# Kernel tuning notes

Hardware: AMD Instinct MI355X
Metric: run time of the kernel (lower is better)

## Reference

```python
import jax, jax.numpy as jnp
import numpy as np

N = 131072   # total inner-graph nodes (G * n)
G = 2048     # number of inner graphs = nodes of outer graph fg
n = 64       # nodes per inner graph (contiguous blocks)
E = 1048576  # inner edges
EF = 32768   # outer (fg) edges
D = 128      # emb_dim == hidden_dim
K = 8        # SortPooling k
VOCAB = 150


def setup_inputs() -> dict:
    key = jax.random.key(0)
    ks = jax.random.split(key, 32)
    p = lambda k, shape: (jax.random.normal(k, shape, jnp.float32) * 0.1)
    inp = {
        'h': jax.random.randint(ks[0], (N,), 0, VOCAB),
        'g_src': jax.random.randint(ks[1], (E,), 0, N),
        'g_dst': jax.random.randint(ks[2], (E,), 0, N),
        'fg_src': jax.random.randint(ks[3], (EF,), 0, G),
        'fg_dst': jax.random.randint(ks[4], (EF,), 0, G),
        'token_emb': p(ks[5], (VOCAB, D)),
        # GATConv 1 (D -> D, 1 head): fc weight (in,out), attn vectors, output bias
        'W1': p(ks[6], (D, D)), 'al1': p(ks[7], (D,)), 'ar1': p(ks[8], (D,)), 'b1': p(ks[9], (D,)),
        # GATConv 2
        'W2': p(ks[10], (D, D)), 'al2': p(ks[11], (D,)), 'ar2': p(ks[12], (D,)), 'b2': p(ks[13], (D,)),
        # GATConv 3 (K*D -> D) over fg
        'W3': p(ks[14], (K * D, D)), 'al3': p(ks[15], (D,)), 'ar3': p(ks[16], (D,)), 'b3': p(ks[17], (D,)),
        # linear_forward
        'Wf': p(ks[18], (D, D)), 'bf': p(ks[19], (D,)),
        # linear
        'Wl': p(ks[20], (D, D)), 'bl': p(ks[21], (D,)),
        # linear1
        'Wl1': p(ks[22], (D, D)), 'bl1': p(ks[23], (D,)),
        # clasifier
        'Wc': p(ks[24], (D, 2)), 'bc': p(ks[25], (2,)),
    }
    return inp


def gat_conv(src, dst, num_nodes, x, W, al, ar, b):
    """DGL GATConv, num_heads=1, allow_zero_in_degree=True, no activation."""
    f = x @ W                                   # [N, D] projected features
    el = f @ al                                 # [N] left attention logits
    er = f @ ar                                 # [N] right attention logits
    e = jax.nn.leaky_relu(el[src] + er[dst], 0.2)   # [E] per-edge score
    m = jax.ops.segment_max(e, dst, num_segments=num_nodes)
    a = jnp.exp(e - m[dst])
    s = jax.ops.segment_sum(a, dst, num_segments=num_nodes)
    alpha = a / s[dst]                          # edge softmax over incoming edges
    out = jax.ops.segment_sum(alpha[:, None] * f[src], dst, num_segments=num_nodes)
    return out + b                              # zero-in-degree nodes -> bias only


def sort_pooling(x, num_graphs, nodes_per_graph, k):
    """DGL SortPooling: sort each node's feature ascending, rank nodes by last
    channel descending, take top-k, concat -> [G, k*D]."""
    d = x.shape[-1]
    x = jnp.sort(x.reshape(num_graphs, nodes_per_graph, d), axis=-1)
    idx = jnp.argsort(-x[:, :, -1], axis=1)[:, :k]          # [G, k]
    topk = jnp.take_along_axis(x, idx[:, :, None], axis=1)  # [G, k, D]
    return topk.reshape(num_graphs, k * d)


def reference(h, g_src, g_dst, fg_src, fg_dst, token_emb,
              W1, al1, ar1, b1, W2, al2, ar2, b2, W3, al3, ar3, b3,
              Wf, bf, Wl, bl, Wl1, bl1, Wc, bc):
    x = jax.nn.relu(token_emb[h])                                   # [N, D]
    x = jax.nn.relu(gat_conv(g_src, g_dst, N, x, W1, al1, ar1, b1))
    x = jax.nn.relu(gat_conv(g_src, g_dst, N, x, W2, al2, ar2, b2))
    x = jax.nn.relu(x @ Wf + bf)                                    # linear_forward
    x = sort_pooling(x, G, n, K)                                    # [G, K*D]
    x = jax.nn.relu(gat_conv(fg_src, fg_dst, G, x, W3, al3, ar3, b3))
    x = jax.nn.relu(x @ Wl + bl)                                    # dropout = eval identity
    x = jax.nn.relu(x @ Wl1 + bl1)
    x = x @ Wc + bc
    return x.reshape(-1, 2)
```

## Files before the change

### kernel.cpp

```cpp
#include <hip/hip_runtime.h>
#include <math.h>

#define NN   131072
#define GG   2048
#define NPG  64
#define EE   1048576
#define EFN  32768
#define DD   128
#define KK   8

typedef unsigned short bfu;
typedef short bf16x8 __attribute__((ext_vector_type(8)));
typedef float f32x4 __attribute__((ext_vector_type(4)));

static __device__ __forceinline__ bfu f2b(float f) {
  unsigned u = __float_as_uint(f);
  u += 0x7FFFu + ((u >> 16) & 1u);
  return (bfu)(u >> 16);
}
static __device__ __forceinline__ float b2f(bfu b) {
  return __uint_as_float(((unsigned)b) << 16);
}

__global__ void fill_f32_kernel(float* __restrict__ p, float v, int nElems) {
  int i = blockIdx.x * 256 + threadIdx.x;
  if (i < nElems) p[i] = v;
}

__global__ void zero_int_kernel(int* __restrict__ p, int nElems) {
  int i = blockIdx.x * 256 + threadIdx.x;
  if (i < nElems) p[i] = 0;
}

__global__ void init_softmax_kernel(float* __restrict__ mx, float* __restrict__ sm, int nElems) {
  int i = blockIdx.x * 256 + threadIdx.x;
  if (i < nElems) { mx[i] = -INFINITY; sm[i] = 0.f; }
}

__global__ void embed_relu_kernel(const float* __restrict__ temb,
                                  const int* __restrict__ h,
                                  float* __restrict__ x, int total) {
  int i = blockIdx.x * 256 + threadIdx.x;
  if (i >= total) return;
  int node = i >> 7, d = i & 127;
  x[i] = fmaxf(temb[h[node] * DD + d], 0.f);
}

template <int KD, int ROWS>
__global__ __launch_bounds__(128) void gemm_kernel(
    const float* __restrict__ A, const float* __restrict__ W,
    const float* __restrict__ bias, float* __restrict__ out,
    int relu_flag) {
  __shared__ float As[ROWS * KD];
  const int row0 = blockIdx.x * ROWS;
  const int tid = threadIdx.x;
  for (int i = tid; i < ROWS * KD; i += 128) As[i] = A[(size_t)row0 * KD + i];
  __syncthreads();
  float acc[ROWS];
#pragma unroll
  for (int r = 0; r < ROWS; r++) acc[r] = 0.f;
  for (int k = 0; k < KD; k++) {
    float w = W[k * 128 + tid];
#pragma unroll
    for (int r = 0; r < ROWS; r++) acc[r] += As[r * KD + k] * w;
  }
  float b = bias ? bias[tid] : 0.f;
#pragma unroll
  for (int r = 0; r < ROWS; r++) {
    float v = acc[r] + b;
    if (relu_flag) v = fmaxf(v, 0.f);
    out[(size_t)(row0 + r) * 128 + tid] = v;
  }
}

__global__ __launch_bounds__(256) void gemm1024_kernel(
    const float* __restrict__ A, const float* __restrict__ W,
    float* __restrict__ out) {
  __shared__ float As[8 * 1024];
  __shared__ float red[8][256];
  const int t = threadIdx.x;
  const int row0 = blockIdx.x * 8;
  for (int idx = t; idx < 8 * 256; idx += 256) {
    int r = idx >> 8, c4 = (idx & 255) << 2;
    *(float4*)&As[r * 1024 + c4] = *(const float4*)(A + (size_t)(row0 + r) * 1024 + c4);
  }
  __syncthreads();
  const int col = t & 127, kh = t >> 7;
  const int k0 = kh * 512;
  float acc[8];
#pragma unroll
  for (int r = 0; r < 8; r++) acc[r] = 0.f;
  for (int k = k0; k < k0 + 512; k += 4) {
    float w0 = W[(size_t)(k + 0) * 128 + col];
    float w1 = W[(size_t)(k + 1) * 128 + col];
    float w2 = W[(size_t)(k + 2) * 128 + col];
    float w3 = W[(size_t)(k + 3) * 128 + col];
#pragma unroll
    for (int r = 0; r < 8; r++) {
      float4 a = *(const float4*)&As[r * 1024 + k];
      acc[r] += a.x * w0 + a.y * w1 + a.z * w2 + a.w * w3;
    }
  }
#pragma unroll
  for (int r = 0; r < 8; r++) red[r][t] = acc[r];
  __syncthreads();
  for (int idx = t; idx < 1024; idx += 256) {
    int r = idx >> 7, c = idx & 127;
    out[(size_t)(row0 + r) * 128 + c] = red[r][c] + red[r][128 + c];
  }
}

__global__ void pack_w_kernel(const float* __restrict__ W,
                              bfu* __restrict__ hi, bfu* __restrict__ lo) {
  int i = blockIdx.x * 256 + threadIdx.x;
  if (i >= 16384) return;
  int k = i >> 7, n = i & 127;
  float w = W[i];
  bfu h = f2b(w);
  bfu l = f2b(w - b2f(h));
  int kk = k >> 5, k5 = k & 31, quad = k5 >> 3, j = k5 & 7;
  int tt = n >> 4, m16 = n & 15;
  int pos = ((((kk * 8 + tt) * 4 + quad) * 16) + m16) * 8 + j;
  hi[pos] = h;
  lo[pos] = l;
}

template <int SRC_MODE, int EPI>
__global__ __launch_bounds__(256) void mfma_gemm(
    const float* A, const float* __restrict__ temb,
    const int* __restrict__ hidx,
    const bfu* __restrict__ WfHi, const bfu* __restrict__ WfLo,
    const float* __restrict__ bias, void* out,
    const float* __restrict__ al, const float* __restrict__ ar,
    float* __restrict__ el, float* __restrict__ er,
    float* __restrict__ keyb) {
  const int t = threadIdx.x;
  const int lane = t & 63, wv_ = t >> 6;
  const int m16 = lane & 15, quad = lane >> 4;
  const int rowbase = blockIdx.x * 64 + wv_ * 16;
  const int grow = rowbase + m16;
  const float* arow = (SRC_MODE == 1) ? (temb + (size_t)hidx[grow] * 128)
                                      : (A + (size_t)grow * 128);
  f32x4 acc[8];
#pragma unroll
  for (int i = 0; i < 8; i++) acc[i] = (f32x4){0.f, 0.f, 0.f, 0.f};
#pragma unroll
  for (int kk = 0; kk < 4; kk++) {
    int k0 = kk * 32 + quad * 8;
    float av[8];
    *(float4*)&av[0] = *(const float4*)(arow + k0);
    *(float4*)&av[4] = *(const float4*)(arow + k0 + 4);
    if (SRC_MODE == 1) {
#pragma unroll
      for (int i = 0; i < 8; i++) av[i] = fmaxf(av[i], 0.f);
    }
    bf16x8 ahi, alo;
#pragma unroll
    for (int i = 0; i < 8; i++) {
      bfu hi = f2b(av[i]);
      bfu lo = f2b(av[i] - b2f(hi));
      ahi[i] = (short)hi;
      alo[i] = (short)lo;
    }
#pragma unroll
    for (int tt = 0; tt < 8; tt++) {
      int pos = ((((kk * 8 + tt) * 4 + quad) * 16) + m16) * 8;
      bf16x8 bhi = *(const bf16x8*)&WfHi[pos];
      bf16x8 blo = *(const bf16x8*)&WfLo[pos];
      acc[tt] = __builtin_amdgcn_mfma_f32_16x16x32_bf16(ahi, bhi, acc[tt], 0, 0, 0);
      acc[tt] = __builtin_amdgcn_mfma_f32_16x16x32_bf16(ahi, blo, acc[tt], 0, 0, 0);
      acc[tt] = __builtin_amdgcn_mfma_f32_16x16x32_bf16(alo, bhi, acc[tt], 0, 0, 0);
    }
  }
  if (EPI == 1) {
    float pl[4] = {0.f, 0.f, 0.f, 0.f}, pr[4] = {0.f, 0.f, 0.f, 0.f};
#pragma unroll
    for (int tt = 0; tt < 8; tt++) {
      int col = tt * 16 + m16;
      float alv = al[col], arv = ar[col];
#pragma unroll
      for (int r = 0; r < 4; r++) {
        float v = acc[tt][r];
        ((bfu*)out)[(size_t)(rowbase + quad * 4 + r) * 128 + col] = f2b(v);
        pl[r] += v * alv;
        pr[r] += v * arv;
      }
    }
#pragma unroll
    for (int r = 0; r < 4; r++) {
      float a0 = pl[r], a1 = pr[r];
#pragma unroll
      for (int off = 1; off < 16; off <<= 1) {
        a0 += __shfl_xor(a0, off);
        a1 += __shfl_xor(a1, off);
      }
      if (m16 == 0) {
        el[rowbase + quad * 4 + r] = a0;
        er[rowbase + quad * 4 + r] = a1;
      }
    }
  } else {
    float pm[4] = {-INFINITY, -INFINITY, -INFINITY, -INFINITY};
#pragma unroll
    for (int tt = 0; tt < 8; tt++) {
      int col = tt * 16 + m16;
      float bv = bias[col];
#pragma unroll
      for (int r = 0; r < 4; r++) {
        float v = fmaxf(acc[tt][r] + bv, 0.f);
        ((float*)out)[(size_t)(rowbase + quad * 4 + r) * 128 + col] = v;
        pm[r] = fmaxf(pm[r], v);
      }
    }
#pragma unroll
    for (int r = 0; r < 4; r++) {
      float a0 = pm[r];
#pragma unroll
      for (int off = 1; off < 16; off <<= 1) a0 = fmaxf(a0, __shfl_xor(a0, off));
      if (m16 == 0) keyb[rowbase + quad * 4 + r] = a0;
    }
  }
}

__global__ __launch_bounds__(64) void attn_logits_kernel(
    const float* __restrict__ f, const float* __restrict__ al,
    const float* __restrict__ ar, float* __restrict__ el,
    float* __restrict__ er) {
  int node = blockIdx.x, lane = threadIdx.x;
  float v1 = f[(size_t)node * 128 + lane];
  float v2 = f[(size_t)node * 128 + 64 + lane];
  float sl = v1 * al[lane] + v2 * al[64 + lane];
  float sr = v1 * ar[lane] + v2 * ar[64 + lane];
#pragma unroll
  for (int off = 32; off; off >>= 1) {
    sl += __shfl_down(sl, off);
    sr += __shfl_down(sr, off);
  }
  if (lane == 0) { el[node] = sl; er[node] = sr; }
}

__global__ void hist_rank_kernel(const int* __restrict__ dst, int* __restrict__ cnt,
                                 int* __restrict__ rank, int nE) {
  int e = blockIdx.x * 256 + threadIdx.x;
  if (e < nE) rank[e] = atomicAdd(&cnt[dst[e]], 1);
}

__global__ __launch_bounds__(256) void scan_block_kernel(
    const int* __restrict__ cnt, int* __restrict__ excl, int* __restrict__ part) {
  __shared__ int s[256];
  int blk = blockIdx.x, tid = threadIdx.x;
  int base = blk * 1024 + tid * 4;
  int a0 = cnt[base], a1 = cnt[base + 1], a2 = cnt[base + 2], a3 = cnt[base + 3];
  int tsum = a0 + a1 + a2 + a3;
  s[tid] = tsum; __syncthreads();
  for (int off = 1; off < 256; off <<= 1) {
    int v = (tid >= off) ? s[tid - off] : 0;
    __syncthreads();
    s[tid] += v;
    __syncthreads();
  }
  int texcl = s[tid] - tsum;
  excl[base]     = texcl;
  excl[base + 1] = texcl + a0;
  excl[base + 2] = texcl + a0 + a1;
  excl[base + 3] = texcl + a0 + a1 + a2;
  if (tid == 255) part[blk] = s[255];
}

__global__ __launch_bounds__(128) void scan_part_kernel(int* __restrict__ part) {
  __shared__ int s[128];
  int tid = threadIdx.x;
  int orig = part[tid];
  s[tid] = orig; __syncthreads();
  for (int off = 1; off < 128; off <<= 1) {
    int v = (tid >= off) ? s[tid - off] : 0;
    __syncthreads();
    s[tid] += v;
    __syncthreads();
  }
  part[tid] = s[tid] - orig;
}

__global__ void scan_add_kernel(int* __restrict__ row_ptr, const int* __restrict__ part,
                                int n, int total) {
  int i = blockIdx.x * 256 + threadIdx.x;
  if (i < n) row_ptr[i] += part[i >> 10];
  if (i == 0) row_ptr[n] = total;
}

__global__ void scatter2_kernel(const int* __restrict__ dst, const int* __restrict__ src,
                                const int* __restrict__ row_ptr, const int* __restrict__ rank,
                                int* __restrict__ adj_src, int nE) {
  int e = blockIdx.x * 256 + threadIdx.x;
  if (e >= nE) return;
  adj_src[row_ptr[dst[e]] + rank[e]] = src[e];
}

__global__ __launch_bounds__(256) void gat_aggregate_csr_kernel(
    const bfu* __restrict__ F, const float* __restrict__ el,
    const float* __restrict__ er, const int* __restrict__ row_ptr,
    const int* __restrict__ adj_src,
    const float* __restrict__ bias, float* __restrict__ outX) {
  const int t = threadIdx.x;
  const int l = t & 31;
  const int gb = t & 32;
  const int d = blockIdx.x * 8 + (t >> 5);
  const int c0 = l * 4;
  int beg = row_ptr[d];
  int n = row_ptr[d + 1] - beg;
  float4 bv = *(const float4*)&bias[c0];
  if (n == 0) {
    float4 o;
    o.x = fmaxf(bv.x, 0.f); o.y = fmaxf(bv.y, 0.f);
    o.z = fmaxf(bv.z, 0.f); o.w = fmaxf(bv.w, 0.f);
    *(float4*)&outX[(size_t)d * 128 + c0] = o;
    return;
  }
  float er_d = er[d];
  float4 acc = make_float4(0.f, 0.f, 0.f, 0.f);
  if (n <= 32) {
    int sv = 0; float sc = -INFINITY;
    if (l < n) {
      sv = adj_src[beg + l];
      float v = el[sv] + er_d;
      sc = v > 0.f ? v : 0.2f * v;
    }
    float m = sc;
#pragma unroll
    for (int off = 16; off; off >>= 1) m = fmaxf(m, __shfl_xor(m, off));
    float ex = (l < n) ? expf(sc - m) : 0.f;
    float s = ex;
#pragma unroll
    for (int off = 16; off; off >>= 1) s += __shfl_xor(s, off);
    float wt = ex / s;
    for (int j = 0; j < n; j += 4) {
      int   s0 = __shfl(sv, gb + j);
      float w0 = __shfl(wt, gb + j);
      int   j1 = (j + 1 < n) ? j + 1 : j;
      int   s1 = __shfl(sv, gb + j1); float w1 = (j + 1 < n) ? __shfl(wt, gb + j1) : 0.f;
      int   j2 = (j + 2 < n) ? j + 2 : j;
      int   s2 = __shfl(sv, gb + j2); float w2 = (j + 2 < n) ? __shfl(wt, gb + j2) : 0.f;
      int   j3 = (j + 3 < n) ? j + 3 : j;
      int   s3 = __shfl(sv, gb + j3); float w3 = (j + 3 < n) ? __shfl(wt, gb + j3) : 0.f;
      ushort4 f0 = *(const ushort4*)&F[(size_t)s0 * 128 + c0];
      ushort4 f1 = *(const ushort4*)&F[(size_t)s1 * 128 + c0];
      ushort4 f2 = *(const ushort4*)&F[(size_t)s2 * 128 + c0];
      ushort4 f3 = *(const ushort4*)&F[(size_t)s3 * 128 + c0];
      acc.x += w0 * b2f(f0.x) + w1 * b2f(f1.x) + w2 * b2f(f2.x) + w3 * b2f(f3.x);
      acc.y += w0 * b2f(f0.y) + w1 * b2f(f1.y) + w2 * b2f(f2.y) + w3 * b2f(f3.y);
      acc.z += w0 * b2f(f0.z) + w1 * b2f(f1.z) + w2 * b2f(f2.z) + w3 * b2f(f3.z);
      acc.w += w0 * b2f(f0.w) + w1 * b2f(f1.w) + w2 * b2f(f2.w) + w3 * b2f(f3.w);
    }
  } else {
    float lm = -INFINITY;
    for (int e = l; e < n; e += 32) {
      int sv = adj_src[beg + e];
      float v = el[sv] + er_d;
      v = v > 0.f ? v : 0.2f * v;
      lm = fmaxf(lm, v);
    }
#pragma unroll
    for (int off = 16; off; off >>= 1) lm = fmaxf(lm, __shfl_xor(lm, off));
    float ls = 0.f;
    for (int e = l; e < n; e += 32) {
      int sv = adj_src[beg + e];
      float v = el[sv] + er_d;
      v = v > 0.f ? v : 0.2f * v;
      ls += expf(v - lm);
    }
#pragma unroll
    for (int off = 16; off; off >>= 1) ls += __shfl_xor(ls, off);
    for (int base = 0; base < n; base += 32) {
      int e = base + l;
      int sv = 0; float wt = 0.f;
      if (e < n) {
        sv = adj_src[beg + e];
        float v = el[sv] + er_d;
        v = v > 0.f ? v : 0.2f * v;
        wt = expf(v - lm) / ls;
      }
      int cnt = min(32, n - base);
      for (int j = 0; j < cnt; ++j) {
        int s0 = __shfl(sv, gb + j);
        float w0 = __shfl(wt, gb + j);
        ushort4 f0 = *(const ushort4*)&F[(size_t)s0 * 128 + c0];
        acc.x += w0 * b2f(f0.x);
        acc.y += w0 * b2f(f0.y);
        acc.z += w0 * b2f(f0.z);
        acc.w += w0 * b2f(f0.w);
      }
    }
  }
  float4 o;
  o.x = fmaxf(acc.x + bv.x, 0.f);
  o.y = fmaxf(acc.y + bv.y, 0.f);
  o.z = fmaxf(acc.z + bv.z, 0.f);
  o.w = fmaxf(acc.w + bv.w, 0.f);
  *(float4*)&outX[(size_t)d * 128 + c0] = o;
}

static __device__ __forceinline__ void atomicMaxF(float* addr, float v) {
  int iv = __float_as_int(v);
  if (iv >= 0) atomicMax((int*)addr, iv);
  else atomicMin((unsigned int*)addr, (unsigned int)iv);
}

static __device__ __forceinline__ float edge_score(const float* el, const float* er,
                                                   int sv, int dv) {
  float v = el[sv] + er[dv];
  return v > 0.f ? v : 0.2f * v;
}

__global__ void edge_max_kernel(const float* __restrict__ el,
                                const float* __restrict__ er,
                                const int* __restrict__ src,
                                const int* __restrict__ dst,
                                float* __restrict__ m, int nE) {
  int e = blockIdx.x * 256 + threadIdx.x;
  if (e >= nE) return;
  atomicMaxF(&m[dst[e]], edge_score(el, er, src[e], dst[e]));
}

__global__ void edge_expsum_kernel(const float* __restrict__ el,
                                   const float* __restrict__ er,
                                   const float* __restrict__ m,
                                   const int* __restrict__ src,
                                   const int* __restrict__ dst,
                                   float* __restrict__ s, int nE) {
  int e = blockIdx.x * 256 + threadIdx.x;
  if (e >= nE) return;
  int d = dst[e];
  atomicAdd(&s[d], expf(edge_score(el, er, src[e], d) - m[d]));
}

__global__ __launch_bounds__(128) void edge_aggregate_kernel(
    const float* __restrict__ f, const float* __restrict__ el,
    const float* __restrict__ er, const float* __restrict__ m,
    const float* __restrict__ s, const int* __restrict__ src,
    const int* __restrict__ dst, float* __restrict__ out, int nE) {
  int e = blockIdx.x;
  int d = threadIdx.x;
  int sv = src[e], dv = dst[e];
  float alpha = expf(edge_score(el, er, sv, dv) - m[dv]) / s[dv];
  atomicAdd(&out[(size_t)dv * 128 + d], alpha * f[(size_t)sv * 128 + d]);
}

__global__ void bias_relu_kernel(float* __restrict__ x,
                                 const float* __restrict__ b, int total) {
  int i = blockIdx.x * 256 + threadIdx.x;
  if (i >= total) return;
  x[i] = fmaxf(x[i] + b[i & 127], 0.f);
}

__global__ __launch_bounds__(64) void row_max_kernel(const float* __restrict__ x,
                                                     float* __restrict__ key) {
  int node = blockIdx.x, lane = threadIdx.x;
  float v = fmaxf(x[(size_t)node * 128 + lane], x[(size_t)node * 128 + 64 + lane]);
#pragma unroll
  for (int off = 32; off; off >>= 1) v = fmaxf(v, __shfl_down(v, off));
  if (lane == 0) key[node] = v;
}

__global__ __launch_bounds__(64) void select_topk_kernel(
    const float* __restrict__ key, int* __restrict__ sel) {
  __shared__ float keys[NPG];
  int g = blockIdx.x, t = threadIdx.x;
  keys[t] = key[(size_t)g * NPG + t];
  __syncthreads();
  float myk = keys[t];
  int rank = 0;
  for (int j = 0; j < NPG; ++j) {
    float kj = keys[j];
    rank += (kj > myk) || (kj == myk && j < t);
  }
  if (rank < KK) sel[g * KK + rank] = t;
}

__global__ __launch_bounds__(128) void sort_rows_kernel(
    const float* __restrict__ x, const int* __restrict__ sel,
    float* __restrict__ xp) {
  __shared__ float v[128];
  int b = blockIdx.x;
  int t = threadIdx.x;
  int g = b >> 3, r = b & 7;
  int node = sel[b];
  v[t] = x[(size_t)(g * NPG + node) * 128 + t];
  __syncthreads();
  for (int k = 2; k <= 128; k <<= 1) {
    for (int j = k >> 1; j > 0; j >>= 1) {
      int ixj = t ^ j;
      if (ixj > t) {
        float a = v[t], bb = v[ixj];
        bool asc = ((t & k) == 0);
        if (asc ? (a > bb) : (a < bb)) { v[t] = bb; v[ixj] = a; }
      }
      __syncthreads();
    }
  }
  xp[(size_t)g * (KK * 128) + r * 128 + t] = v[t];
}

__global__ __launch_bounds__(128) void mlp_tail_kernel(
    const float* __restrict__ g3, const float* __restrict__ Wl,
    const float* __restrict__ bl, const float* __restrict__ Wl1,
    const float* __restrict__ bl1, const float* __restrict__ Wc,
    const float* __restrict__ bc, float* __restrict__ out) {
  __shared__ float buf[128];
  __shared__ float r0[128], r1[128];
  int g = blockIdx.x, t = threadIdx.x;
  buf[t] = g3[(size_t)g * 128 + t];
  __syncthreads();
  float a = 0.f;
  for (int k = 0; k < 128; k++) a += buf[k] * Wl[k * 128 + t];
  float t1 = fmaxf(a + bl[t], 0.f);
  __syncthreads();
  buf[t] = t1;
  __syncthreads();
  a = 0.f;
  for (int k = 0; k < 128; k++) a += buf[k] * Wl1[k * 128 + t];
  float t2 = fmaxf(a + bl1[t], 0.f);
  r0[t] = t2 * Wc[t * 2 + 0];
  r1[t] = t2 * Wc[t * 2 + 1];
  __syncthreads();
  for (int off = 64; off; off >>= 1) {
    if (t < off) { r0[t] += r0[t + off]; r1[t] += r1[t + off]; }
    __syncthreads();
  }
  if (t == 0) {
    out[g * 2 + 0] = r0[0] + bc[0];
    out[g * 2 + 1] = r1[0] + bc[1];
  }
}

extern "C" void kernel_launch(void* const* d_in, const int* in_sizes, int n_in,
                              void* d_out, int out_size, void* d_ws, size_t ws_size,
                              hipStream_t stream) {
  const size_t BASE_FLOATS = (size_t)NN * DD * 2 + (size_t)NN * 4;
  const size_t CSR_INTS = (size_t)(NN + 1) + NN + EE + 128;
  if (ws_size < BASE_FLOATS * sizeof(float)) {
    hipMemsetAsync(d_out, 0, (size_t)out_size * sizeof(float), stream);
    return;
  }
  const bool use_csr = ws_size >= BASE_FLOATS * sizeof(float) + CSR_INTS * sizeof(int);

  const int* h      = (const int*)d_in[0];
  const int* g_src  = (const int*)d_in[1];
  const int* g_dst  = (const int*)d_in[2];
  const int* fg_src = (const int*)d_in[3];
  const int* fg_dst = (const int*)d_in[4];
  const float* temb = (const float*)d_in[5];
  const float* W1 = (const float*)d_in[6];
  const float* al1 = (const float*)d_in[7];
  const float* ar1 = (const float*)d_in[8];
  const float* b1 = (const float*)d_in[9];
  const float* W2 = (const float*)d_in[10];
  const float* al2 = (const float*)d_in[11];
  const float* ar2 = (const float*)d_in[12];
  const float* b2 = (const float*)d_in[13];
  const float* W3 = (const float*)d_in[14];
  const float* al3 = (const float*)d_in[15];
  const float* ar3 = (const float*)d_in[16];
  const float* b3 = (const float*)d_in[17];
  const float* Wf = (const float*)d_in[18];
  const float* bfv = (const float*)d_in[19];
  const float* Wl = (const float*)d_in[20];
  const float* bl = (const float*)d_in[21];
  const float* Wl1 = (const float*)d_in[22];
  const float* bl1 = (const float*)d_in[23];
  const float* Wc = (const float*)d_in[24];
  const float* bc = (const float*)d_in[25];
  float* out = (float*)d_out;

  float* ws = (float*)d_ws;
  float* X  = ws;
  float* F  = X + (size_t)NN * DD;
  float* el = F + (size_t)NN * DD;
  float* er = el + NN;
  float* mx = er + NN;
  float* sm = mx + NN;
  int* row_ptr = (int*)(sm + NN);
  int* cursor  = row_ptr + NN + 1;
  int* adj_src = cursor + NN;
  int* part    = adj_src + EE;
  int* rankb = (int*)X;
  bfu* w1h = (bfu*)mx;
  bfu* w1l = w1h + 16384;
  bfu* w2h = w1l + 16384;
  bfu* w2l = w2h + 16384;
  bfu* wfh = w2l + 16384;
  bfu* wfl = wfh + 16384;
  float* xp   = F;
  float* f3   = F + 2097152;
  float* g3   = f3 + (size_t)GG * DD;
  float* t1   = g3 + (size_t)GG * DD;
  float* t2   = t1 + (size_t)GG * DD;
  float* keyb = t2 + (size_t)GG * DD;
  int*   sel  = (int*)(keyb + NN);

  const int totalND = NN * DD;

  if (use_csr) {
    bfu* Fb = (bfu*)F;
    zero_int_kernel<<<NN / 256, 256, 0, stream>>>(cursor, NN);
    hist_rank_kernel<<<EE / 256, 256, 0, stream>>>(g_dst, cursor, rankb, EE);
    scan_block_kernel<<<NN / 1024, 256, 0, stream>>>(cursor, row_ptr, part);
    scan_part_kernel<<<1, 128, 0, stream>>>(part);
    scan_add_kernel<<<(NN + 255) / 256, 256, 0, stream>>>(row_ptr, part, NN, EE);
    scatter2_kernel<<<EE / 256, 256, 0, stream>>>(g_dst, g_src, row_ptr, rankb, adj_src, EE);

    pack_w_kernel<<<64, 256, 0, stream>>>(W1, w1h, w1l);
    pack_w_kernel<<<64, 256, 0, stream>>>(W2, w2h, w2l);
    pack_w_kernel<<<64, 256, 0, stream>>>(Wf, wfh, wfl);

    mfma_gemm<1, 1><<<NN / 64, 256, 0, stream>>>(
        nullptr, temb, h, w1h, w1l, nullptr, Fb, al1, ar1, el, er, nullptr);
    gat_aggregate_csr_kernel<<<NN / 8, 256, 0, stream>>>(Fb, el, er, row_ptr, adj_src, b1, X);

    mfma_gemm<0, 1><<<NN / 64, 256, 0, stream>>>(
        X, nullptr, nullptr, w2h, w2l, nullptr, Fb, al2, ar2, el, er, nullptr);
    gat_aggregate_csr_kernel<<<NN / 8, 256, 0, stream>>>(Fb, el, er, row_ptr, adj_src, b2, X);

    mfma_gemm<0, 2><<<NN / 64, 256, 0, stream>>>(
        X, nullptr, nullptr, wfh, wfl, bfv, X, nullptr, nullptr, nullptr, nullptr, keyb);
  } else {
    embed_relu_kernel<<<totalND / 256, 256, 0, stream>>>(temb, h, X, totalND);
    auto gat_inner = [&](const float* W, const float* al, const float* ar, const float* bb) {
      gemm_kernel<DD, 8><<<NN / 8, 128, 0, stream>>>(X, W, nullptr, F, 0);
      attn_logits_kernel<<<NN, 64, 0, stream>>>(F, al, ar, el, er);
      init_softmax_kernel<<<(NN + 255) / 256, 256, 0, stream>>>(mx, sm, NN);
      fill_f32_kernel<<<totalND / 256, 256, 0, stream>>>(X, 0.f, totalND);
      edge_max_kernel<<<(EE + 255) / 256, 256, 0, stream>>>(el, er, g_src, g_dst, mx, EE);
      edge_expsum_kernel<<<(EE + 255) / 256, 256, 0, stream>>>(el, er, mx, g_src, g_dst, sm, EE);
      edge_aggregate_kernel<<<EE, 128, 0, stream>>>(F, el, er, mx, sm, g_src, g_dst, X, EE);
      bias_relu_kernel<<<totalND / 256, 256, 0, stream>>>(X, bb, totalND);
    };
    gat_inner(W1, al1, ar1, b1);
    gat_inner(W2, al2, ar2, b2);
    gemm_kernel<DD, 8><<<NN / 8, 128, 0, stream>>>(X, Wf, bfv, X, 1);
    row_max_kernel<<<NN, 64, 0, stream>>>(X, keyb);
  }

  select_topk_kernel<<<GG, 64, 0, stream>>>(keyb, sel);
  sort_rows_kernel<<<GG * KK, 128, 0, stream>>>(X, sel, xp);

  gemm1024_kernel<<<GG / 8, 256, 0, stream>>>(xp, W3, f3);
  attn_logits_kernel<<<GG, 64, 0, stream>>>(f3, al3, ar3, el, er);
  init_softmax_kernel<<<(GG + 255) / 256, 256, 0, stream>>>(mx, sm, GG);
  fill_f32_kernel<<<(GG * DD + 255) / 256, 256, 0, stream>>>(g3, 0.f, GG * DD);
  edge_max_kernel<<<(EFN + 255) / 256, 256, 0, stream>>>(el, er, fg_src, fg_dst, mx, EFN);
  edge_expsum_kernel<<<(EFN + 255) / 256, 256, 0, stream>>>(el, er, mx, fg_src, fg_dst, sm, EFN);
  edge_aggregate_kernel<<<EFN, 128, 0, stream>>>(f3, el, er, mx, sm, fg_src, fg_dst, g3, EFN);
  bias_relu_kernel<<<(GG * DD + 255) / 256, 256, 0, stream>>>(g3, b3, GG * DD);

  mlp_tail_kernel<<<GG, 128, 0, stream>>>(g3, Wl, bl, Wl1, bl1, Wc, bc, out);
}
```

Before: 479.1 us.

## Use CSR softmax aggregation for outer graph and widen MFMA GEMM row tile

The outer-graph GAT now builds a CSR by destination (histogram, single-block scan, scatter) and runs a fused per-destination softmax-and-aggregate kernel. This replaces the atomic edge max, expsum and per-edge aggregate kernels along with the zero-fill and bias passes. Separately, the MFMA GEMM now processes 32 rows per wave instead of 16, so each loaded weight fragment is reused twice. The cost is higher register pressure and half as many blocks.

```diff
diff --git a/kernel.cpp b/kernel.cpp
--- a/kernel.cpp
+++ b/kernel.cpp
@@ -137,87 +137,104 @@
   const int t = threadIdx.x;
   const int lane = t & 63, wv_ = t >> 6;
   const int m16 = lane & 15, quad = lane >> 4;
-  const int rowbase = blockIdx.x * 64 + wv_ * 16;
-  const int grow = rowbase + m16;
-  const float* arow = (SRC_MODE == 1) ? (temb + (size_t)hidx[grow] * 128)
-                                      : (A + (size_t)grow * 128);
-  f32x4 acc[8];
-#pragma unroll
-  for (int i = 0; i < 8; i++) acc[i] = (f32x4){0.f, 0.f, 0.f, 0.f};
+  const int rowbase = blockIdx.x * 128 + wv_ * 32;
+  const float* arow0 = (SRC_MODE == 1) ? (temb + (size_t)hidx[rowbase + m16] * 128)
+                                       : (A + (size_t)(rowbase + m16) * 128);
+  const float* arow1 = (SRC_MODE == 1) ? (temb + (size_t)hidx[rowbase + 16 + m16] * 128)
+                                       : (A + (size_t)(rowbase + 16 + m16) * 128);
+  f32x4 acc[2][8];
+#pragma unroll
+  for (int rg = 0; rg < 2; rg++)
+#pragma unroll
+    for (int i = 0; i < 8; i++) acc[rg][i] = (f32x4){0.f, 0.f, 0.f, 0.f};
 #pragma unroll
   for (int kk = 0; kk < 4; kk++) {
     int k0 = kk * 32 + quad * 8;
-    float av[8];
-    *(float4*)&av[0] = *(const float4*)(arow + k0);
-    *(float4*)&av[4] = *(const float4*)(arow + k0 + 4);
+    float av0[8], av1[8];
+    *(float4*)&av0[0] = *(const float4*)(arow0 + k0);
+    *(float4*)&av0[4] = *(const float4*)(arow0 + k0 + 4);
+    *(float4*)&av1[0] = *(const float4*)(arow1 + k0);
+    *(float4*)&av1[4] = *(const float4*)(arow1 + k0 + 4);
     if (SRC_MODE == 1) {
 #pragma unroll
-      for (int i = 0; i < 8; i++) av[i] = fmaxf(av[i], 0.f);
-    }
-    bf16x8 ahi, alo;
+      for (int i = 0; i < 8; i++) {
+        av0[i] = fmaxf(av0[i], 0.f);
+        av1[i] = fmaxf(av1[i], 0.f);
+      }
+    }
+    bf16x8 ahi0, alo0, ahi1, alo1;
 #pragma unroll
     for (int i = 0; i < 8; i++) {
-      bfu hi = f2b(av[i]);
-      bfu lo = f2b(av[i] - b2f(hi));
-      ahi[i] = (short)hi;
-      alo[i] = (short)lo;
+      bfu h0 = f2b(av0[i]);
+      alo0[i] = (short)f2b(av0[i] - b2f(h0));
+      ahi0[i] = (short)h0;
+      bfu h1 = f2b(av1[i]);
+      alo1[i] = (short)f2b(av1[i] - b2f(h1));
+      ahi1[i] = (short)h1;
     }
 #pragma unroll
     for (int tt = 0; tt < 8; tt++) {
       int pos = ((((kk * 8 + tt) * 4 + quad) * 16) + m16) * 8;
       bf16x8 bhi = *(const bf16x8*)&WfHi[pos];
       bf16x8 blo = *(const bf16x8*)&WfLo[pos];
-      acc[tt] = __builtin_amdgcn_mfma_f32_16x16x32_bf16(ahi, bhi, acc[tt], 0, 0, 0);
-      acc[tt] = __builtin_amdgcn_mfma_f32_16x16x32_bf16(ahi, blo, acc[tt], 0, 0, 0);
-      acc[tt] = __builtin_amdgcn_mfma_f32_16x16x32_bf16(alo, bhi, acc[tt], 0, 0, 0);
-    }
-  }
-  if (EPI == 1) {
-    float pl[4] = {0.f, 0.f, 0.f, 0.f}, pr[4] = {0.f, 0.f, 0.f, 0.f};
-#pragma unroll
-    for (int tt = 0; tt < 8; tt++) {
-      int col = tt * 16 + m16;
-      float alv = al[col], arv = ar[col];
+      acc[0][tt] = __builtin_amdgcn_mfma_f32_16x16x32_bf16(ahi0, bhi, acc[0][tt], 0, 0, 0);
+      acc[0][tt] = __builtin_amdgcn_mfma_f32_16x16x32_bf16(ahi0, blo, acc[0][tt], 0, 0, 0);
+      acc[0][tt] = __builtin_amdgcn_mfma_f32_16x16x32_bf16(alo0, bhi, acc[0][tt], 0, 0, 0);
+      acc[1][tt] = __builtin_amdgcn_mfma_f32_16x16x32_bf16(ahi1, bhi, acc[1][tt], 0, 0, 0);
+      acc[1][tt] = __builtin_amdgcn_mfma_f32_16x16x32_bf16(ahi1, blo, acc[1][tt], 0, 0, 0);
+      acc[1][tt] = __builtin_amdgcn_mfma_f32_16x16x32_bf16(alo1, bhi, acc[1][tt], 0, 0, 0);
+    }
+  }
+#pragma unroll
+  for (int rg = 0; rg < 2; rg++) {
+    const int rb = rowbase + rg * 16;
+    if (EPI == 1) {
+      float pl[4] = {0.f, 0.f, 0.f, 0.f}, pr[4] = {0.f, 0.f, 0.f, 0.f};
+#pragma unroll
+      for (int tt = 0; tt < 8; tt++) {
+        int col = tt * 16 + m16;
+        float alv = al[col], arv = ar[col];
+#pragma unroll
+        for (int r = 0; r < 4; r++) {
+          float v = acc[rg][tt][r];
+          ((bfu*)out)[(size_t)(rb + quad * 4 + r) * 128 + col] = f2b(v);
+          pl[r] += v * alv;
+          pr[r] += v * arv;
+        }
+      }
 #pragma unroll
       for (int r = 0; r < 4; r++) {
-        float v = acc[tt][r];
-        ((bfu*)out)[(size_t)(rowbase + quad * 4 + r) * 128 + col] = f2b(v);
-        pl[r] += v * alv;
-        pr[r] += v * arv;
-      }
-    }
-#pragma unroll
-    for (int r = 0; r < 4; r++) {
-      float a0 = pl[r], a1 = pr[r];
-#pragma unroll
-      for (int off = 1; off < 16; off <<= 1) {
-        a0 += __shfl_xor(a0, off);
-        a1 += __shfl_xor(a1, off);
-      }
-      if (m16 == 0) {
-        el[rowbase + quad * 4 + r] = a0;
-        er[rowbase + quad * 4 + r] = a1;
-      }
-    }
-  } else {
-    float pm[4] = {-INFINITY, -INFINITY, -INFINITY, -INFINITY};
-#pragma unroll
-    for (int tt = 0; tt < 8; tt++) {
-      int col = tt * 16 + m16;
-      float bv = bias[col];
+        float a0 = pl[r], a1 = pr[r];
+#pragma unroll
+        for (int off = 1; off < 16; off <<= 1) {
+          a0 += __shfl_xor(a0, off);
+          a1 += __shfl_xor(a1, off);
+        }
+        if (m16 == 0) {
+          el[rb + quad * 4 + r] = a0;
+          er[rb + quad * 4 + r] = a1;
+        }
+      }
+    } else {
+      float pm[4] = {-INFINITY, -INFINITY, -INFINITY, -INFINITY};
+#pragma unroll
+      for (int tt = 0; tt < 8; tt++) {
+        int col = tt * 16 + m16;
+        float bv = bias[col];
+#pragma unroll
+        for (int r = 0; r < 4; r++) {
+          float v = fmaxf(acc[rg][tt][r] + bv, 0.f);
+          ((float*)out)[(size_t)(rb + quad * 4 + r) * 128 + col] = v;
+          pm[r] = fmaxf(pm[r], v);
+        }
+      }
 #pragma unroll
       for (int r = 0; r < 4; r++) {
-        float v = fmaxf(acc[tt][r] + bv, 0.f);
-        ((float*)out)[(size_t)(rowbase + quad * 4 + r) * 128 + col] = v;
-        pm[r] = fmaxf(pm[r], v);
-      }
-    }
-#pragma unroll
-    for (int r = 0; r < 4; r++) {
-      float a0 = pm[r];
-#pragma unroll
-      for (int off = 1; off < 16; off <<= 1) a0 = fmaxf(a0, __shfl_xor(a0, off));
-      if (m16 == 0) keyb[rowbase + quad * 4 + r] = a0;
+        float a0 = pm[r];
+#pragma unroll
+        for (int off = 1; off < 16; off <<= 1) a0 = fmaxf(a0, __shfl_xor(a0, off));
+        if (m16 == 0) keyb[rb + quad * 4 + r] = a0;
+      }
     }
   }
 }
@@ -286,6 +303,28 @@
   int i = blockIdx.x * 256 + threadIdx.x;
   if (i < n) row_ptr[i] += part[i >> 10];
   if (i == 0) row_ptr[n] = total;
+}
+
+__global__ __launch_bounds__(256) void scan2048_kernel(const int* __restrict__ cnt,
+                                                       int* __restrict__ rp, int total) {
+  __shared__ int s[256];
+  int t = threadIdx.x;
+  int base = t * 8;
+  int v[8];
+  int tsum = 0;
+#pragma unroll
+  for (int i = 0; i < 8; i++) { v[i] = cnt[base + i]; tsum += v[i]; }
+  s[t] = tsum; __syncthreads();
+  for (int off = 1; off < 256; off <<= 1) {
+    int x = (t >= off) ? s[t - off] : 0;
+    __syncthreads();
+    s[t] += x;
+    __syncthreads();
+  }
+  int excl = s[t] - tsum;
+#pragma unroll
+  for (int i = 0; i < 8; i++) { rp[base + i] = excl; excl += v[i]; }
+  if (t == 255) rp[2048] = total;
 }
 
 __global__ void scatter2_kernel(const int* __restrict__ dst, const int* __restrict__ src,
@@ -397,6 +436,96 @@
   o.z = fmaxf(acc.z + bv.z, 0.f);
   o.w = fmaxf(acc.w + bv.w, 0.f);
   *(float4*)&outX[(size_t)d * 128 + c0] = o;
+}
+
+__global__ __launch_bounds__(256) void gat_aggregate_outer_kernel(
+    const float* __restrict__ F, const float* __restrict__ el,
+    const float* __restrict__ er, const int* __restrict__ row_ptr,
+    const int* __restrict__ adj_src,
+    const float* __restrict__ bias, float* __restrict__ outG) {
+  const int t = threadIdx.x;
+  const int l = t & 31;
+  const int gb = t & 32;
+  const int d = blockIdx.x * 8 + (t >> 5);
+  const int c0 = l * 4;
+  int beg = row_ptr[d];
+  int n = row_ptr[d + 1] - beg;
+  float4 bv = *(const float4*)&bias[c0];
+  if (n == 0) {
+    float4 o;
+    o.x = fmaxf(bv.x, 0.f); o.y = fmaxf(bv.y, 0.f);
+    o.z = fmaxf(bv.z, 0.f); o.w = fmaxf(bv.w, 0.f);
+    *(float4*)&outG[(size_t)d * 128 + c0] = o;
+    return;
+  }
+  float er_d = er[d];
+  float4 acc = make_float4(0.f, 0.f, 0.f, 0.f);
+  if (n <= 32) {
+    int sv = 0; float sc = -INFINITY;
+    if (l < n) {
+      sv = adj_src[beg + l];
+      float v = el[sv] + er_d;
+      sc = v > 0.f ? v : 0.2f * v;
+    }
+    float m = sc;
+#pragma unroll
+    for (int off = 16; off; off >>= 1) m = fmaxf(m, __shfl_xor(m, off));
+    float ex = (l < n) ? expf(sc - m) : 0.f;
+    float s = ex;
+#pragma unroll
+    for (int off = 16; off; off >>= 1) s += __shfl_xor(s, off);
+    float wt = ex / s;
+    for (int j = 0; j < n; ++j) {
+      int   s0 = __shfl(sv, gb + j);
+      float w0 = __shfl(wt, gb + j);
+      float4 f0 = *(const float4*)&F[(size_t)s0 * 128 + c0];
+      acc.x += w0 * f0.x; acc.y += w0 * f0.y;
+      acc.z += w0 * f0.z; acc.w += w0 * f0.w;
+    }
+  } else {
+    float lm = -INFINITY;
+    for (int e = l; e < n; e += 32) {
+      int sv = adj_src[beg + e];
+      float v = el[sv] + er_d;
+      v = v > 0.f ? v : 0.2f * v;
+      lm = fmaxf(lm, v);
+    }
+#pragma unroll
+    for (int off = 16; off; off >>= 1) lm = fmaxf(lm, __shfl_xor(lm, off));
+    float ls = 0.f;
+    for (int e = l; e < n; e += 32) {
+      int sv = adj_src[beg + e];
+      float v = el[sv] + er_d;
+      v = v > 0.f ? v : 0.2f * v;
+      ls += expf(v - lm);
+    }
+#pragma unroll
+    for (int off = 16; off; off >>= 1) ls += __shfl_xor(ls, off);
+    for (int base = 0; base < n; base += 32) {
+      int e = base + l;
+      int sv = 0; float wt = 0.f;
+      if (e < n) {
+        sv = adj_src[beg + e];
+        float v = el[sv] + er_d;
+        v = v > 0.f ? v : 0.2f * v;
+        wt = expf(v - lm) / ls;
+      }
+      int cnt = min(32, n - base);
+      for (int j = 0; j < cnt; ++j) {
+        int s0 = __shfl(sv, gb + j);
+        float w0 = __shfl(wt, gb + j);
+        float4 f0 = *(const float4*)&F[(size_t)s0 * 128 + c0];
+        acc.x += w0 * f0.x; acc.y += w0 * f0.y;
+        acc.z += w0 * f0.z; acc.w += w0 * f0.w;
+      }
+    }
+  }
+  float4 o;
+  o.x = fmaxf(acc.x + bv.x, 0.f);
+  o.y = fmaxf(acc.y + bv.y, 0.f);
+  o.z = fmaxf(acc.z + bv.z, 0.f);
+  o.w = fmaxf(acc.w + bv.w, 0.f);
+  *(float4*)&outG[(size_t)d * 128 + c0] = o;
 }
 
 static __device__ __forceinline__ void atomicMaxF(float* addr, float v) {
@@ -589,6 +718,10 @@
   bfu* w2l = w2h + 16384;
   bfu* wfh = w2l + 16384;
   bfu* wfl = wfh + 16384;
+  int* ocnt  = (int*)X;
+  int* orp   = ocnt + 2048;
+  int* orank = orp + 2080;
+  int* oadj  = orank + EFN;
   float* xp   = F;
   float* f3   = F + 2097152;
   float* g3   = f3 + (size_t)GG * DD;
@@ -612,16 +745,29 @@
     pack_w_kernel<<<64, 256, 0, stream>>>(W2, w2h, w2l);
     pack_w_kernel<<<64, 256, 0, stream>>>(Wf, wfh, wfl);
 
-    mfma_gemm<1, 1><<<NN / 64, 256, 0, stream>>>(
+    mfma_gemm<1, 1><<<NN / 128, 256, 0, stream>>>(
         nullptr, temb, h, w1h, w1l, nullptr, Fb, al1, ar1, el, er, nullptr);
     gat_aggregate_csr_kernel<<<NN / 8, 256, 0, stream>>>(Fb, el, er, row_ptr, adj_src, b1, X);
 
-    mfma_gemm<0, 1><<<NN / 64, 256, 0, stream>>>(
+    mfma_gemm<0, 1><<<NN / 128, 256, 0, stream>>>(
         X, nullptr, nullptr, w2h, w2l, nullptr, Fb, al2, ar2, el, er, nullptr);
     gat_aggregate_csr_kernel<<<NN / 8, 256, 0, stream>>>(Fb, el, er, row_ptr, adj_src, b2, X);
 
-    mfma_gemm<0, 2><<<NN / 64, 256, 0, stream>>>(
+    mfma_gemm<0, 2><<<NN / 128, 256, 0, stream>>>(
         X, nullptr, nullptr, wfh, wfl, bfv, X, nullptr, nullptr, nullptr, nullptr, keyb);
+
+    select_topk_kernel<<<GG, 64, 0, stream>>>(keyb, sel);
+    sort_rows_kernel<<<GG * KK, 128, 0, stream>>>(X, sel, xp);
+
+    gemm1024_kernel<<<GG / 8, 256, 0, stream>>>(xp, W3, f3);
+    attn_logits_kernel<<<GG, 64, 0, stream>>>(f3, al3, ar3, el, er);
+    zero_int_kernel<<<GG / 256, 256, 0, stream>>>(ocnt, GG);
+    hist_rank_kernel<<<EFN / 256, 256, 0, stream>>>(fg_dst, ocnt, orank, EFN);
+    scan2048_kernel<<<1, 256, 0, stream>>>(ocnt, orp, EFN);
+    scatter2_kernel<<<EFN / 256, 256, 0, stream>>>(fg_dst, fg_src, orp, orank, oadj, EFN);
+    gat_aggregate_outer_kernel<<<GG / 8, 256, 0, stream>>>(f3, el, er, orp, oadj, b3, g3);
+
+    mlp_tail_kernel<<<GG, 128, 0, stream>>>(g3, Wl, bl, Wl1, bl1, Wc, bc, out);
   } else {
     embed_relu_kernel<<<totalND / 256, 256, 0, stream>>>(temb, h, X, totalND);
     auto gat_inner = [&](const float* W, const float* al, const float* ar, const float* bb) {
@@ -638,19 +784,18 @@
     gat_inner(W2, al2, ar2, b2);
     gemm_kernel<DD, 8><<<NN / 8, 128, 0, stream>>>(X, Wf, bfv, X, 1);
     row_max_kernel<<<NN, 64, 0, stream>>>(X, keyb);
-  }
-
-  select_topk_kernel<<<GG, 64, 0, stream>>>(keyb, sel);
-  sort_rows_kernel<<<GG * KK, 128, 0, stream>>>(X, sel, xp);
-
-  gemm1024_kernel<<<GG / 8, 256, 0, stream>>>(xp, W3, f3);
-  attn_logits_kernel<<<GG, 64, 0, stream>>>(f3, al3, ar3, el, er);
-  init_softmax_kernel<<<(GG + 255) / 256, 256, 0, stream>>>(mx, sm, GG);
-  fill_f32_kernel<<<(GG * DD + 255) / 256, 256, 0, stream>>>(g3, 0.f, GG * DD);
-  edge_max_kernel<<<(EFN + 255) / 256, 256, 0, stream>>>(el, er, fg_src, fg_dst, mx, EFN);
-  edge_expsum_kernel<<<(EFN + 255) / 256, 256, 0, stream>>>(el, er, mx, fg_src, fg_dst, sm, EFN);
-  edge_aggregate_kernel<<<EFN, 128, 0, stream>>>(f3, el, er, mx, sm, fg_src, fg_dst, g3, EFN);
-  bias_relu_kernel<<<(GG * DD + 255) / 256, 256, 0, stream>>>(g3, b3, GG * DD);
-
-  mlp_tail_kernel<<<GG, 128, 0, stream>>>(g3, Wl, bl, Wl1, bl1, Wc, bc, out);
-}
+
+    select_topk_kernel<<<GG, 64, 0, stream>>>(keyb, sel);
+    sort_rows_kernel<<<GG * KK, 128, 0, stream>>>(X, sel, xp);
+
+    gemm1024_kernel<<<GG / 8, 256, 0, stream>>>(xp, W3, f3);
+    attn_logits_kernel<<<GG, 64, 0, stream>>>(f3, al3, ar3, el, er);
+    init_softmax_kernel<<<(GG + 255) / 256, 256, 0, stream>>>(mx, sm, GG);
+    fill_f32_kernel<<<(GG * DD + 255) / 256, 256, 0, stream>>>(g3, 0.f, GG * DD);
+    edge_max_kernel<<<(EFN + 255) / 256, 256, 0, stream>>>(el, er, fg_src, fg_dst, mx, EFN);
+    edge_expsum_kernel<<<(EFN + 255) / 256, 256, 0, stream>>>(el, er, mx, fg_src, fg_dst, sm, EFN);
+    edge_aggregate_kernel<<<EFN, 128, 0, stream>>>(f3, el, er, mx, sm, fg_src, fg_dst, g3, EFN);
+    bias_relu_kernel<<<(GG * DD + 255) / 256, 256, 0, stream>>>(g3, b3, GG * DD);
+    mlp_tail_kernel<<<GG, 128, 0, stream>>>(g3, Wl, bl, Wl1, bl1, Wc, bc, out);
+  }
+}
```

Result: faster. 468.8 us, median of 2 (-2.1%).
